# Optimization experiments

Measured on AMD Instinct MI355X. Metric: run time of the kernel, lower is better.

## Reference

```python
import jax, jax.numpy as jnp
import numpy as np

SAMPLING_RATIO = 1.0


def gcn_conv(x, src, dst, ew, W, b):
    """PyG GCNConv: h = D^-1/2 (A+I) D^-1/2 (xW) + b, edges weighted by ew.
    Masked edges (ew=0) contribute neither messages nor degree, exactly
    matching running the conv on the subset edge_index."""
    n = x.shape[0]
    h = x @ W                                              # [N, out]
    deg = jax.ops.segment_sum(ew, dst, num_segments=n) + 1.0  # +1 for self-loop
    dinv = jax.lax.rsqrt(deg)                              # deg >= 1, safe
    norm = dinv[src] * dinv[dst] * ew                      # [E]
    agg = jax.ops.segment_sum(h[src] * norm[:, None], dst, num_segments=n)
    return agg + h * (dinv * dinv)[:, None] + b            # self-loop term + bias


def setup_inputs() -> dict:
    key = jax.random.key(0)
    ks = jax.random.split(key, 8)
    N, E, F_IN, HID, OUT = 50000, 800000, 128, 128, 64
    x = jax.random.normal(ks[0], (N, F_IN), dtype=jnp.float32)
    edge_index = jax.random.randint(ks[1], (2, E), 0, N, dtype=jnp.int32)
    edge_rand = jax.random.uniform(ks[2], (E,), dtype=jnp.float32)
    s0 = 1.0 / np.sqrt(F_IN)
    s1 = 1.0 / np.sqrt(HID)
    w0 = jax.random.normal(ks[3], (F_IN, HID), dtype=jnp.float32) * s0
    b0 = jnp.zeros((HID,), dtype=jnp.float32)
    w1 = jax.random.normal(ks[4], (HID, HID), dtype=jnp.float32) * s1
    b1 = jnp.zeros((HID,), dtype=jnp.float32)
    w2 = jax.random.normal(ks[5], (HID, OUT), dtype=jnp.float32) * s1
    b2 = jnp.zeros((OUT,), dtype=jnp.float32)
    return {"x": x, "edge_index": edge_index, "edge_rand": edge_rand,
            "w0": w0, "b0": b0, "w1": w1, "b1": b1, "w2": w2, "b2": b2}


def reference(x, edge_index, edge_rand, w0, b0, w1, b1, w2, b2):
    src, dst = edge_index[0], edge_index[1]
    ones = jnp.ones(src.shape, dtype=x.dtype)
    # first pass over full graph -> tmp_z
    z = jax.nn.relu(gcn_conv(x, src, dst, ones, w0, b0))
    z = jax.nn.relu(gcn_conv(z, src, dst, ones, w1, b1))
    tmp_z = gcn_conv(z, src, dst, ones, w2, b2)
    # edge sampling: gather-dot-sigmoid-threshold (detached mask)
    edge_logit = jnp.sum(tmp_z[src] * tmp_z[dst], axis=-1)
    edge_weight = jax.nn.sigmoid(edge_logit)
    mask = jax.lax.stop_gradient(
        (edge_weight > SAMPLING_RATIO * edge_rand).astype(x.dtype))
    # second pass: sampled edges for hidden layers, full edges for last layer
    h = jax.nn.relu(gcn_conv(x, src, dst, mask, w0, b0))
    h = jax.nn.relu(gcn_conv(h, src, dst, mask, w1, b1))
    out = gcn_conv(h, src, dst, ones, w2, b2)
    return out
```

## Files before the change

kernel.cpp:

```cpp
#include <hip/hip_runtime.h>


typedef __attribute__((ext_vector_type(8))) short bf16x8;
typedef __attribute__((ext_vector_type(4))) float f32x4;

__device__ inline unsigned bfpair(float lo, float hi) {
    unsigned a = __float_as_uint(lo), b = __float_as_uint(hi);
    a = (a + 0x7FFFu + ((a >> 16) & 1u)) >> 16;
    b = (b + 0x7FFFu + ((b >> 16) & 1u)) & 0xFFFF0000u;
    return a | b;
}
__device__ inline unsigned short bf1(float v) {
    unsigned u = __float_as_uint(v);
    return (unsigned short)((u + 0x7FFFu + ((u >> 16) & 1u)) >> 16);
}
__device__ inline void unpack2(unsigned u, float& f0, float& f1) {
    f0 = __uint_as_float(u << 16);
    f1 = __uint_as_float(u & 0xFFFF0000u);
}

__global__ void k_scan1(const int* __restrict__ in, int* __restrict__ out,
                        int* __restrict__ bsums, int N) {
    __shared__ int tmp[256];
    int i = blockIdx.x * 256 + threadIdx.x;
    int v = (i < N) ? in[i] : 0;
    tmp[threadIdx.x] = v;
    __syncthreads();
    for (int off = 1; off < 256; off <<= 1) {
        int t = (threadIdx.x >= off) ? tmp[threadIdx.x - off] : 0;
        __syncthreads();
        tmp[threadIdx.x] += t;
        __syncthreads();
    }
    if (i < N) out[i] = tmp[threadIdx.x] - v;
    if (threadIdx.x == 255) bsums[blockIdx.x] = tmp[255];
}

__global__ void k_scan2(int* __restrict__ bsums, int nb) {
    __shared__ int tmp[256];
    int v = (threadIdx.x < nb) ? bsums[threadIdx.x] : 0;
    tmp[threadIdx.x] = v;
    __syncthreads();
    for (int off = 1; off < 256; off <<= 1) {
        int t = (threadIdx.x >= off) ? tmp[threadIdx.x - off] : 0;
        __syncthreads();
        tmp[threadIdx.x] += t;
        __syncthreads();
    }
    if (threadIdx.x < nb) bsums[threadIdx.x] = tmp[threadIdx.x] - v;
}

__global__ void k_scan3(int* __restrict__ out, const int* __restrict__ bsums, int N, int E) {
    int i = blockIdx.x * 256 + threadIdx.x;
    if (i < N) out[i] += bsums[blockIdx.x];
    if (i == 0) out[N] = E;
}

__global__ __launch_bounds__(256) void k_bcount(const int* __restrict__ dst,
                                                int* __restrict__ cnt, int E, int chunk) {
    __shared__ int h[1024];
    for (int i = threadIdx.x; i < 1024; i += 256) h[i] = 0;
    __syncthreads();
    int beg = blockIdx.x * chunk, end = min(E, beg + chunk);
    for (int e = beg + threadIdx.x; e < end; e += 256)
        atomicAdd(&h[dst[e] >> 6], 1);
    __syncthreads();
    for (int b = threadIdx.x; b < 1024; b += 256)
        cnt[b * 64 + blockIdx.x] = h[b];
}

__global__ __launch_bounds__(256) void k_bscatter(const int* __restrict__ src,
                                                  const int* __restrict__ dst,
                                                  const float* __restrict__ er,
                                                  const int* __restrict__ sbase,
                                                  int2* __restrict__ stg, int E, int chunk) {
    __shared__ int cur[1024];
    for (int i = threadIdx.x; i < 1024; i += 256) cur[i] = 0;
    __syncthreads();
    int beg = blockIdx.x * chunk, end = min(E, beg + chunk);
    for (int e = beg + threadIdx.x; e < end; e += 256) {
        int d = dst[e];
        int b = d >> 6;
        int loc = atomicAdd(&cur[b], 1);
        int pos = sbase[b * 64 + blockIdx.x] + loc;
        stg[pos] = make_int2(src[e] | ((d & 63) << 16), (int)__float_as_uint(er[e]));
    }
}

__global__ __launch_bounds__(256) void k_bindeg(const int2* __restrict__ stg,
                                                const int* __restrict__ sbase,
                                                int* __restrict__ indeg,
                                                float* __restrict__ dinvF, int N) {
    __shared__ int cnt[64];
    if (threadIdx.x < 64) cnt[threadIdx.x] = 0;
    __syncthreads();
    int b = blockIdx.x;
    int beg = sbase[b * 64], end = sbase[(b + 1) * 64];
    for (int i = beg + threadIdx.x; i < end; i += 256)
        atomicAdd(&cnt[(stg[i].x >> 16) & 63], 1);
    __syncthreads();
    if (threadIdx.x < 64) {
        int node = b * 64 + threadIdx.x;
        if (node < N) {
            int c = cnt[threadIdx.x];
            indeg[node] = c;
            dinvF[node] = 1.0f / sqrtf((float)c + 1.0f);
        }
    }
}

__global__ __launch_bounds__(256) void k_bfill(const int2* __restrict__ stg,
                                               const int* __restrict__ sbase,
                                               const int* __restrict__ csr_off,
                                               int2* __restrict__ csr_se, int N) {
    __shared__ int cur[64];
    int b = blockIdx.x;
    if (threadIdx.x < 64) {
        int node = b * 64 + threadIdx.x;
        cur[threadIdx.x] = (node < N) ? csr_off[node] : 0;
    }
    __syncthreads();
    int beg = sbase[b * 64], end = sbase[(b + 1) * 64];
    for (int i = beg + threadIdx.x; i < end; i += 256) {
        int2 se = stg[i];
        int j = (se.x >> 16) & 63;
        int pos = atomicAdd(&cur[j], 1);
        csr_se[pos] = make_int2(se.x & 0xFFFF, se.y);
    }
}

__global__ __launch_bounds__(128) void k_surv(const float* __restrict__ tz,
                                              const int* __restrict__ csr_off,
                                              const int2* __restrict__ csr_se,
                                              float* __restrict__ survive,
                                              float* __restrict__ dinvM, int N) {
    const int v = blockIdx.x;
    const int l = threadIdx.x & 15;
    const int s = threadIdx.x >> 4;
    const int e0 = csr_off[v];
    const int e1 = csr_off[v + 1];
    const float4 tv = *(const float4*)&tz[(size_t)v * 64 + l * 4];
    int cnt = 0;
    for (int i = e0 + s; i < e1; i += 8) {
        int2 se = csr_se[i];
        const float4 a = *(const float4*)&tz[(size_t)se.x * 64 + l * 4];
        float p = a.x * tv.x + a.y * tv.y + a.z * tv.z + a.w * tv.w;
        p += __shfl_xor(p, 1, 16);
        p += __shfl_xor(p, 2, 16);
        p += __shfl_xor(p, 4, 16);
        p += __shfl_xor(p, 8, 16);
        float sg = 1.0f / (1.0f + expf(-p));
        float m = (sg > __uint_as_float((unsigned)se.y)) ? 1.0f : 0.0f;
        if (l == 0) {
            survive[i] = m;
            cnt += (m != 0.0f) ? 1 : 0;
        }
    }
    __shared__ int sc[8];
    if (l == 0) sc[s] = cnt;
    __syncthreads();
    if (threadIdx.x == 0) {
        int t = 0;
#pragma unroll
        for (int k = 0; k < 8; k++) t += sc[k];
        dinvM[v] = 1.0f / sqrtf((float)t + 1.0f);
    }
}

__device__ inline void packw3_one(const float* __restrict__ W, unsigned short* __restrict__ Wp,
                                  int OUTC, int idx) {
    int l = idx & 63;
    int tk = idx >> 6;
    int kb = tk & 3;
    int ct = tk >> 2;
    size_t PL = (size_t)(OUTC / 16) * 4 * 64 * 8;
    unsigned short v0[8], v1[8], v2[8];
#pragma unroll
    for (int i = 0; i < 8; i++) {
        float wv = W[(kb * 32 + ((l >> 4) * 8) + i) * OUTC + ct * 16 + (l & 15)];
        unsigned short h0 = bf1(wv);
        float f0 = __uint_as_float((unsigned)h0 << 16);
        float r1 = wv - f0;
        unsigned short h1 = bf1(r1);
        float f1 = __uint_as_float((unsigned)h1 << 16);
        unsigned short h2 = bf1(r1 - f1);
        v0[i] = h0; v1[i] = h1; v2[i] = h2;
    }
    auto st = [](unsigned short* dst, unsigned short* v) {
        uint4 u;
        u.x = v[0] | ((unsigned)v[1] << 16);
        u.y = v[2] | ((unsigned)v[3] << 16);
        u.z = v[4] | ((unsigned)v[5] << 16);
        u.w = v[6] | ((unsigned)v[7] << 16);
        *(uint4*)dst = u;
    };
    st(&Wp[(size_t)idx * 8], v0);
    st(&Wp[PL + (size_t)idx * 8], v1);
    st(&Wp[2 * PL + (size_t)idx * 8], v2);
}

__global__ void k_packw3_all(const float* __restrict__ w0, const float* __restrict__ w1,
                             const float* __restrict__ w2,
                             unsigned short* __restrict__ w0p, unsigned short* __restrict__ w1p,
                             unsigned short* __restrict__ w2p) {
    int b = blockIdx.x;
    if (b < 8) packw3_one(w0, w0p, 128, b * 256 + threadIdx.x);
    else if (b < 16) packw3_one(w1, w1p, 128, (b - 8) * 256 + threadIdx.x);
    else packw3_one(w2, w2p, 64, (b - 16) * 256 + threadIdx.x);
}

template <int OUTC, bool WB16>
__global__ __launch_bounds__(256) void k_gemm_split(const float* __restrict__ A,
                                                    const unsigned short* __restrict__ Wp,
                                                    float* __restrict__ Cout,
                                                    unsigned short* __restrict__ Cb, int N) {
    constexpr int CT = OUTC / 16;
    constexpr int PL = CT * 4 * 64 * 8;
    constexpr int LDW = OUTC + 4;
    __shared__ float eps[64 * LDW];
    const int w = threadIdx.x >> 6;
    const int l = threadIdx.x & 63;
    int row = blockIdx.x * 64 + w * 16 + (l & 15);
    int rowc = (row < N) ? row : (N - 1);

    bf16x8 a0[4], a1[4], a2[4];
#pragma unroll
    for (int kb = 0; kb < 4; kb++) {
        const float* pa = &A[(size_t)rowc * 128 + kb * 32 + ((l >> 4) * 8)];
        float4 x0 = *(const float4*)pa;
        float4 x1 = *(const float4*)(pa + 4);
        float xa[8] = {x0.x, x0.y, x0.z, x0.w, x1.x, x1.y, x1.z, x1.w};
#pragma unroll
        for (int i = 0; i < 8; i++) {
            unsigned short h0 = bf1(xa[i]);
            float f0 = __uint_as_float((unsigned)h0 << 16);
            float r1 = xa[i] - f0;
            unsigned short h1 = bf1(r1);
            float f1 = __uint_as_float((unsigned)h1 << 16);
            unsigned short h2 = bf1(r1 - f1);
            a0[kb][i] = (short)h0;
            a1[kb][i] = (short)h1;
            a2[kb][i] = (short)h2;
        }
    }
#pragma unroll
    for (int ct = 0; ct < CT; ct++) {
        f32x4 accA = {0.f, 0.f, 0.f, 0.f};
        f32x4 accB = {0.f, 0.f, 0.f, 0.f};
#pragma unroll
        for (int kb = 0; kb < 4; kb++) {
            const size_t bo = ((size_t)(ct * 4 + kb) * 64 + l) * 8;
            bf16x8 b0 = *(const bf16x8*)&Wp[bo];
            bf16x8 b1 = *(const bf16x8*)&Wp[PL + bo];
            bf16x8 b2 = *(const bf16x8*)&Wp[2 * PL + bo];
            accA = __builtin_amdgcn_mfma_f32_16x16x32_bf16(a0[kb], b0, accA, 0, 0, 0);
            accB = __builtin_amdgcn_mfma_f32_16x16x32_bf16(a0[kb], b1, accB, 0, 0, 0);
            accA = __builtin_amdgcn_mfma_f32_16x16x32_bf16(a1[kb], b0, accA, 0, 0, 0);
            accB = __builtin_amdgcn_mfma_f32_16x16x32_bf16(a1[kb], b1, accB, 0, 0, 0);
            accA = __builtin_amdgcn_mfma_f32_16x16x32_bf16(a2[kb], b0, accA, 0, 0, 0);
            accB = __builtin_amdgcn_mfma_f32_16x16x32_bf16(a0[kb], b2, accB, 0, 0, 0);
        }
#pragma unroll
        for (int r = 0; r < 4; r++) {
            int rr = w * 16 + (l >> 4) * 4 + r;
            eps[rr * LDW + ct * 16 + (l & 15)] = accA[r] + accB[r];
        }
    }
    __syncthreads();
    constexpr int NF4 = 64 * OUTC / 4;
    for (int idx = threadIdx.x; idx < NF4; idx += 256) {
        int rl = idx / (OUTC / 4);
        int cg = idx % (OUTC / 4);
        int grow = blockIdx.x * 64 + rl;
        if (grow < N) {
            const float* sp = &eps[rl * LDW + cg * 4];
            float4 vv = make_float4(sp[0], sp[1], sp[2], sp[3]);
            *(float4*)&Cout[(size_t)grow * OUTC + cg * 4] = vv;
            if (WB16)
                *(uint2*)&Cb[(size_t)grow * OUTC + cg * 4] =
                    make_uint2(bfpair(vv.x, vv.y), bfpair(vv.z, vv.w));
        }
    }
}

template <int OUTC>
__global__ __launch_bounds__(256) void k_gemm_mfma(const unsigned short* __restrict__ A,
                                                   const unsigned short* __restrict__ Wpk,
                                                   unsigned short* __restrict__ C, int N) {
    constexpr int CT = OUTC / 16;
    __shared__ unsigned short eps[64 * OUTC];
    const int w = threadIdx.x >> 6;
    const int l = threadIdx.x & 63;
    const int rowl = (w * 16) + (l & 15);
    int row = blockIdx.x * 64 + rowl;
    int rowc = (row < N) ? row : (N - 1);

    bf16x8 a[4];
#pragma unroll
    for (int kb = 0; kb < 4; kb++)
        a[kb] = *(const bf16x8*)&A[(size_t)rowc * 128 + kb * 32 + ((l >> 4) * 8)];

#pragma unroll
    for (int ct = 0; ct < CT; ct++) {
        f32x4 acc = {0.f, 0.f, 0.f, 0.f};
#pragma unroll
        for (int kb = 0; kb < 4; kb++) {
            bf16x8 b = *(const bf16x8*)&Wpk[((size_t)(ct * 4 + kb) * 64 + l) * 8];
            acc = __builtin_amdgcn_mfma_f32_16x16x32_bf16(a[kb], b, acc, 0, 0, 0);
        }
#pragma unroll
        for (int r = 0; r < 4; r++) {
            int rr = w * 16 + (l >> 4) * 4 + r;
            eps[rr * OUTC + ct * 16 + (l & 15)] = bf1(acc[r]);
        }
    }
    __syncthreads();
    constexpr int NU4 = 64 * OUTC / 8;
    for (int idx = threadIdx.x; idx < NU4; idx += 256) {
        int rl = idx / (OUTC / 8);
        int cg = idx % (OUTC / 8);
        int grow = blockIdx.x * 64 + rl;
        if (grow < N)
            *(uint4*)&C[(size_t)grow * OUTC + cg * 8] = *(const uint4*)&eps[rl * OUTC + cg * 8];
    }
}

template <bool RELU>
__global__ __launch_bounds__(256) void k_agg128(const float* __restrict__ h,
                                                const int* __restrict__ csr_off,
                                                const int2* __restrict__ csr_se,
                                                const float* __restrict__ dinv,
                                                const float* __restrict__ bias,
                                                float* __restrict__ out, int N) {
    const int v = blockIdx.x * 4 + (threadIdx.x >> 6);
    if (v >= N) return;
    const int lane = threadIdx.x & 63;
    const int l = lane & 31;
    const int s = lane >> 5;
    const int e0 = csr_off[v];
    const int e1 = csr_off[v + 1];
    float4 acc = make_float4(0.f, 0.f, 0.f, 0.f);
    int i = e0 + s;
    for (; i + 2 < e1; i += 4) {
        int sa = csr_se[i].x;      float wa = dinv[sa];
        int sb = csr_se[i + 2].x;  float wb = dinv[sb];
        float4 a = *(const float4*)&h[(size_t)sa * 128 + l * 4];
        float4 b = *(const float4*)&h[(size_t)sb * 128 + l * 4];
        acc.x = fmaf(a.x, wa, acc.x); acc.y = fmaf(a.y, wa, acc.y);
        acc.z = fmaf(a.z, wa, acc.z); acc.w = fmaf(a.w, wa, acc.w);
        acc.x = fmaf(b.x, wb, acc.x); acc.y = fmaf(b.y, wb, acc.y);
        acc.z = fmaf(b.z, wb, acc.z); acc.w = fmaf(b.w, wb, acc.w);
    }
    if (i < e1) {
        int sa = csr_se[i].x;
        float wa = dinv[sa];
        float4 a = *(const float4*)&h[(size_t)sa * 128 + l * 4];
        acc.x = fmaf(a.x, wa, acc.x); acc.y = fmaf(a.y, wa, acc.y);
        acc.z = fmaf(a.z, wa, acc.z); acc.w = fmaf(a.w, wa, acc.w);
    }
    acc.x += __shfl_xor(acc.x, 32);
    acc.y += __shfl_xor(acc.y, 32);
    acc.z += __shfl_xor(acc.z, 32);
    acc.w += __shfl_xor(acc.w, 32);
    if (s == 0) {
        float dv = dinv[v];
        float4 hv = *(const float4*)&h[(size_t)v * 128 + l * 4];
        float4 bb = *(const float4*)&bias[l * 4];
        float4 o;
        o.x = dv * (acc.x + hv.x * dv) + bb.x;
        o.y = dv * (acc.y + hv.y * dv) + bb.y;
        o.z = dv * (acc.z + hv.z * dv) + bb.z;
        o.w = dv * (acc.w + hv.w * dv) + bb.w;
        if (RELU) {
            o.x = fmaxf(o.x, 0.f); o.y = fmaxf(o.y, 0.f);
            o.z = fmaxf(o.z, 0.f); o.w = fmaxf(o.w, 0.f);
        }
        *(float4*)&out[(size_t)v * 128 + l * 4] = o;
    }
}

__global__ __launch_bounds__(256) void k_agg64(const float* __restrict__ h,
                                               const int* __restrict__ csr_off,
                                               const int2* __restrict__ csr_se,
                                               const float* __restrict__ dinv,
                                               const float* __restrict__ bias,
                                               float* __restrict__ out, int N) {
    const int v = blockIdx.x * 4 + (threadIdx.x >> 6);
    if (v >= N) return;
    const int lane = threadIdx.x & 63;
    const int l = lane & 15;
    const int s = lane >> 4;
    const int e0 = csr_off[v];
    const int e1 = csr_off[v + 1];
    float4 acc = make_float4(0.f, 0.f, 0.f, 0.f);
    int i = e0 + s;
    for (; i + 4 < e1; i += 8) {
        int sa = csr_se[i].x;      float wa = dinv[sa];
        int sb = csr_se[i + 4].x;  float wb = dinv[sb];
        float4 a = *(const float4*)&h[(size_t)sa * 64 + l * 4];
        float4 b = *(const float4*)&h[(size_t)sb * 64 + l * 4];
        acc.x = fmaf(a.x, wa, acc.x); acc.y = fmaf(a.y, wa, acc.y);
        acc.z = fmaf(a.z, wa, acc.z); acc.w = fmaf(a.w, wa, acc.w);
        acc.x = fmaf(b.x, wb, acc.x); acc.y = fmaf(b.y, wb, acc.y);
        acc.z = fmaf(b.z, wb, acc.z); acc.w = fmaf(b.w, wb, acc.w);
    }
    if (i < e1) {
        int sa = csr_se[i].x;
        float wa = dinv[sa];
        float4 a = *(const float4*)&h[(size_t)sa * 64 + l * 4];
        acc.x = fmaf(a.x, wa, acc.x); acc.y = fmaf(a.y, wa, acc.y);
        acc.z = fmaf(a.z, wa, acc.z); acc.w = fmaf(a.w, wa, acc.w);
    }
    acc.x += __shfl_xor(acc.x, 32); acc.y += __shfl_xor(acc.y, 32);
    acc.z += __shfl_xor(acc.z, 32); acc.w += __shfl_xor(acc.w, 32);
    acc.x += __shfl_xor(acc.x, 16); acc.y += __shfl_xor(acc.y, 16);
    acc.z += __shfl_xor(acc.z, 16); acc.w += __shfl_xor(acc.w, 16);
    if (s == 0) {
        float dv = dinv[v];
        float4 hv = *(const float4*)&h[(size_t)v * 64 + l * 4];
        float4 bb = *(const float4*)&bias[l * 4];
        float4 o;
        o.x = dv * (acc.x + hv.x * dv) + bb.x;
        o.y = dv * (acc.y + hv.y * dv) + bb.y;
        o.z = dv * (acc.z + hv.z * dv) + bb.z;
        o.w = dv * (acc.w + hv.w * dv) + bb.w;
        *(float4*)&out[(size_t)v * 64 + l * 4] = o;
    }
}

template <bool RELU>
__global__ __launch_bounds__(256) void k_agg128b(const unsigned short* __restrict__ h,
                                                 const int* __restrict__ csr_off,
                                                 const int2* __restrict__ csr_se,
                                                 const float* __restrict__ survive,
                                                 const float* __restrict__ dinv,
                                                 const float* __restrict__ bias,
                                                 unsigned short* __restrict__ out, int N) {
    const int v = blockIdx.x * 4 + (threadIdx.x >> 6);
    if (v >= N) return;
    const int lane = threadIdx.x & 63;
    const int l = lane & 15;
    const int s = lane >> 4;
    const int e0 = csr_off[v];
    const int e1 = csr_off[v + 1];
    float acc[8];
#pragma unroll
    for (int j = 0; j < 8; j++) acc[j] = 0.f;
    int i = e0 + s;
    for (; i + 4 < e1; i += 8) {
        int sa = csr_se[i].x;
        int sb = csr_se[i + 4].x;
        float wa = dinv[sa] * survive[i];
        float wb = dinv[sb] * survive[i + 4];
        uint4 ua = *(const uint4*)&h[(size_t)sa * 128 + l * 8];
        uint4 ub = *(const uint4*)&h[(size_t)sb * 128 + l * 8];
        float f0, f1;
        unpack2(ua.x, f0, f1); acc[0] = fmaf(f0, wa, acc[0]); acc[1] = fmaf(f1, wa, acc[1]);
        unpack2(ua.y, f0, f1); acc[2] = fmaf(f0, wa, acc[2]); acc[3] = fmaf(f1, wa, acc[3]);
        unpack2(ua.z, f0, f1); acc[4] = fmaf(f0, wa, acc[4]); acc[5] = fmaf(f1, wa, acc[5]);
        unpack2(ua.w, f0, f1); acc[6] = fmaf(f0, wa, acc[6]); acc[7] = fmaf(f1, wa, acc[7]);
        unpack2(ub.x, f0, f1); acc[0] = fmaf(f0, wb, acc[0]); acc[1] = fmaf(f1, wb, acc[1]);
        unpack2(ub.y, f0, f1); acc[2] = fmaf(f0, wb, acc[2]); acc[3] = fmaf(f1, wb, acc[3]);
        unpack2(ub.z, f0, f1); acc[4] = fmaf(f0, wb, acc[4]); acc[5] = fmaf(f1, wb, acc[5]);
        unpack2(ub.w, f0, f1); acc[6] = fmaf(f0, wb, acc[6]); acc[7] = fmaf(f1, wb, acc[7]);
    }
    if (i < e1) {
        int sa = csr_se[i].x;
        float wa = dinv[sa] * survive[i];
        uint4 ua = *(const uint4*)&h[(size_t)sa * 128 + l * 8];
        float f0, f1;
        unpack2(ua.x, f0, f1); acc[0] = fmaf(f0, wa, acc[0]); acc[1] = fmaf(f1, wa, acc[1]);
        unpack2(ua.y, f0, f1); acc[2] = fmaf(f0, wa, acc[2]); acc[3] = fmaf(f1, wa, acc[3]);
        unpack2(ua.z, f0, f1); acc[4] = fmaf(f0, wa, acc[4]); acc[5] = fmaf(f1, wa, acc[5]);
        unpack2(ua.w, f0, f1); acc[6] = fmaf(f0, wa, acc[6]); acc[7] = fmaf(f1, wa, acc[7]);
    }
#pragma unroll
    for (int j = 0; j < 8; j++) acc[j] += __shfl_xor(acc[j], 32);
#pragma unroll
    for (int j = 0; j < 8; j++) acc[j] += __shfl_xor(acc[j], 16);
    if (s == 0) {
        float dv = dinv[v];
        uint4 uh = *(const uint4*)&h[(size_t)v * 128 + l * 8];
        float hv[8];
        unpack2(uh.x, hv[0], hv[1]); unpack2(uh.y, hv[2], hv[3]);
        unpack2(uh.z, hv[4], hv[5]); unpack2(uh.w, hv[6], hv[7]);
        unsigned u[4];
#pragma unroll
        for (int j2 = 0; j2 < 4; j2++) {
            float o0 = dv * (acc[2 * j2 + 0] + hv[2 * j2 + 0] * dv) + bias[l * 8 + 2 * j2 + 0];
            float o1 = dv * (acc[2 * j2 + 1] + hv[2 * j2 + 1] * dv) + bias[l * 8 + 2 * j2 + 1];
            if (RELU) { o0 = fmaxf(o0, 0.f); o1 = fmaxf(o1, 0.f); }
            u[j2] = bfpair(o0, o1);
        }
        *(uint4*)&out[(size_t)v * 128 + l * 8] = make_uint4(u[0], u[1], u[2], u[3]);
    }
}

__global__ __launch_bounds__(256) void k_agg64b(const unsigned short* __restrict__ h,
                                                const int* __restrict__ csr_off,
                                                const int2* __restrict__ csr_se,
                                                const float* __restrict__ dinv,
                                                const float* __restrict__ bias,
                                                float* __restrict__ out, int N) {
    const int v = blockIdx.x * 4 + (threadIdx.x >> 6);
    if (v >= N) return;
    const int lane = threadIdx.x & 63;
    const int l = lane & 7;
    const int s = lane >> 3;
    const int e0 = csr_off[v];
    const int e1 = csr_off[v + 1];
    float acc[8];
#pragma unroll
    for (int j = 0; j < 8; j++) acc[j] = 0.f;
    for (int i = e0 + s; i < e1; i += 8) {
        int sa = csr_se[i].x;
        float wa = dinv[sa];
        uint4 ua = *(const uint4*)&h[(size_t)sa * 64 + l * 8];
        float f0, f1;
        unpack2(ua.x, f0, f1); acc[0] = fmaf(f0, wa, acc[0]); acc[1] = fmaf(f1, wa, acc[1]);
        unpack2(ua.y, f0, f1); acc[2] = fmaf(f0, wa, acc[2]); acc[3] = fmaf(f1, wa, acc[3]);
        unpack2(ua.z, f0, f1); acc[4] = fmaf(f0, wa, acc[4]); acc[5] = fmaf(f1, wa, acc[5]);
        unpack2(ua.w, f0, f1); acc[6] = fmaf(f0, wa, acc[6]); acc[7] = fmaf(f1, wa, acc[7]);
    }
#pragma unroll
    for (int j = 0; j < 8; j++) acc[j] += __shfl_xor(acc[j], 32);
#pragma unroll
    for (int j = 0; j < 8; j++) acc[j] += __shfl_xor(acc[j], 16);
#pragma unroll
    for (int j = 0; j < 8; j++) acc[j] += __shfl_xor(acc[j], 8);
    if (s == 0) {
        float dv = dinv[v];
        uint4 uh = *(const uint4*)&h[(size_t)v * 64 + l * 8];
        float hv[8];
        unpack2(uh.x, hv[0], hv[1]); unpack2(uh.y, hv[2], hv[3]);
        unpack2(uh.z, hv[4], hv[5]); unpack2(uh.w, hv[6], hv[7]);
        float o[8];
#pragma unroll
        for (int j = 0; j < 8; j++) o[j] = dv * (acc[j] + hv[j] * dv) + bias[l * 8 + j];
        *(float4*)&out[(size_t)v * 64 + l * 8 + 0] = make_float4(o[0], o[1], o[2], o[3]);
        *(float4*)&out[(size_t)v * 64 + l * 8 + 4] = make_float4(o[4], o[5], o[6], o[7]);
    }
}

extern "C" void kernel_launch(void* const* d_in, const int* in_sizes, int n_in,
                              void* d_out, int out_size, void* d_ws, size_t ws_size,
                              hipStream_t stream) {
    const float* x  = (const float*)d_in[0];
    const int*   ei = (const int*)d_in[1];
    const float* er = (const float*)d_in[2];
    const float* w0 = (const float*)d_in[3];
    const float* b0 = (const float*)d_in[4];
    const float* w1 = (const float*)d_in[5];
    const float* b1 = (const float*)d_in[6];
    const float* w2 = (const float*)d_in[7];
    const float* b2 = (const float*)d_in[8];
    const int N = in_sizes[0] / 128;
    const int E = in_sizes[2];
    const int* src  = ei;
    const int* dstv = ei + E;
    float* out = (float*)d_out;

    char* p = (char*)d_ws;
    auto alloc = [&](size_t bytes) {
        char* r = p;
        p += (bytes + 255) & ~(size_t)255;
        return r;
    };
    int* indeg     = (int*)alloc((size_t)N * 4);
    int* csr_off   = (int*)alloc((size_t)(N + 1) * 4);
    int* bsums     = (int*)alloc(1024);
    int* bcnt      = (int*)alloc((size_t)65536 * 4);
    int* sbase     = (int*)alloc((size_t)65537 * 4);
    int2* csr_se   = (int2*)alloc((size_t)E * 8);
    int2* stg      = (int2*)alloc((size_t)E * 8);
    float* dinvF   = (float*)alloc((size_t)N * 4);
    float* dinvM   = (float*)alloc((size_t)N * 4);
    float* hx      = (float*)alloc((size_t)N * 128 * 4);
    unsigned short* hxb = (unsigned short*)alloc((size_t)N * 128 * 2);
    float* wk1     = (float*)alloc((size_t)N * 128 * 4);
    float* wk2     = (float*)alloc((size_t)N * 128 * 4);
    float* tz      = (float*)alloc((size_t)N * 64 * 4);
    unsigned short* w0p3 = (unsigned short*)alloc((size_t)3 * 128 * 128 * 2);
    unsigned short* w1p3 = (unsigned short*)alloc((size_t)3 * 128 * 128 * 2);
    unsigned short* w2p3 = (unsigned short*)alloc((size_t)3 * 128 * 64 * 2);
    unsigned short* wk1b = (unsigned short*)wk1;
    unsigned short* wk2b = (unsigned short*)wk2;
    float* survive = (float*)stg;

    const int nb = (N + 255) / 256;
    const int chunk = (E + 63) / 64;

    k_packw3_all<<<20, 256, 0, stream>>>(w0, w1, w2, w0p3, w1p3, w2p3);

    k_bcount<<<64, 256, 0, stream>>>(dstv, bcnt, E, chunk);
    k_scan1<<<256, 256, 0, stream>>>(bcnt, sbase, bsums, 65536);
    k_scan2<<<1, 256, 0, stream>>>(bsums, 256);
    k_scan3<<<256, 256, 0, stream>>>(sbase, bsums, 65536, E);
    k_bscatter<<<64, 256, 0, stream>>>(src, dstv, er, sbase, stg, E, chunk);
    k_bindeg<<<1024, 256, 0, stream>>>(stg, sbase, indeg, dinvF, N);
    k_scan1<<<nb, 256, 0, stream>>>(indeg, csr_off, bsums, N);
    k_scan2<<<1, 256, 0, stream>>>(bsums, nb);
    k_scan3<<<nb, 256, 0, stream>>>(csr_off, bsums, N, E);
    k_bfill<<<1024, 256, 0, stream>>>(stg, sbase, csr_off, csr_se, N);

    const int gbm = (N + 63) / 64;
    const int ga = (N + 3) / 4;

    k_gemm_split<128, true><<<gbm, 256, 0, stream>>>(x, w0p3, hx, hxb, N);

    k_agg128<true><<<ga, 256, 0, stream>>>(hx, csr_off, csr_se, dinvF, b0, wk1, N);
    k_gemm_split<128, false><<<gbm, 256, 0, stream>>>(wk1, w1p3, wk2, nullptr, N);
    k_agg128<true><<<ga, 256, 0, stream>>>(wk2, csr_off, csr_se, dinvF, b1, wk1, N);
    k_gemm_split<64, false><<<gbm, 256, 0, stream>>>(wk1, w2p3, wk2, nullptr, N);
    k_agg64<<<ga, 256, 0, stream>>>(wk2, csr_off, csr_se, dinvF, b2, tz, N);

    k_surv<<<N, 128, 0, stream>>>(tz, csr_off, csr_se, survive, dinvM, N);

    k_agg128b<true><<<ga, 256, 0, stream>>>(hxb, csr_off, csr_se, survive, dinvM, b0, wk1b, N);
    k_gemm_mfma<128><<<gbm, 256, 0, stream>>>(wk1b, w1p3, wk2b, N);
    k_agg128b<true><<<ga, 256, 0, stream>>>(wk2b, csr_off, csr_se, survive, dinvM, b1, wk1b, N);
    k_gemm_mfma<64><<<gbm, 256, 0, stream>>>(wk1b, w2p3, wk2b, N);
    k_agg64b<<<ga, 256, 0, stream>>>(wk2b, csr_off, csr_se, dinvF, b2, out, N);
}
```

Measured before the change: 462.5 us.

## Store node features in 16-column slices to improve gather cache locality

Changes intermediate feature matrices to a sliced layout where each group of 16 columns is stored contiguously for all nodes. Aggregation kernels are replaced by generic sliced kernels that launch one block per (node group, slice), gathering only a 64-byte (or 32-byte bf16) piece per neighbor. This shrinks the working set each slice touches so neighbor gathers hit L2/MALL more often. In exchange it multiplies grid size and repeats CSR/dinv reads per slice, and uses many more smaller random loads.

```diff
diff --git a/kernel.cpp b/kernel.cpp
--- a/kernel.cpp
+++ b/kernel.cpp
@@ -209,7 +209,7 @@
     else packw3_one(w2, w2p, 64, (b - 16) * 256 + threadIdx.x);
 }
 
-template <int OUTC, bool WB16>
+template <int OUTC, bool WB16, bool ASL>
 __global__ __launch_bounds__(256) void k_gemm_split(const float* __restrict__ A,
                                                     const unsigned short* __restrict__ Wp,
                                                     float* __restrict__ Cout,
@@ -226,7 +226,9 @@
     bf16x8 a0[4], a1[4], a2[4];
 #pragma unroll
     for (int kb = 0; kb < 4; kb++) {
-        const float* pa = &A[(size_t)rowc * 128 + kb * 32 + ((l >> 4) * 8)];
+        int col0 = kb * 32 + ((l >> 4) * 8);
+        const float* pa = ASL ? &A[((size_t)(col0 >> 4) * N + rowc) * 16 + (col0 & 15)]
+                              : &A[(size_t)rowc * 128 + col0];
         float4 x0 = *(const float4*)pa;
         float4 x1 = *(const float4*)(pa + 4);
         float xa[8] = {x0.x, x0.y, x0.z, x0.w, x1.x, x1.y, x1.z, x1.w};
@@ -275,10 +277,11 @@
         if (grow < N) {
             const float* sp = &eps[rl * LDW + cg * 4];
             float4 vv = make_float4(sp[0], sp[1], sp[2], sp[3]);
-            *(float4*)&Cout[(size_t)grow * OUTC + cg * 4] = vv;
+            int col0 = cg * 4;
+            size_t ad = ((size_t)(col0 >> 4) * N + grow) * 16 + (col0 & 15);
+            *(float4*)&Cout[ad] = vv;
             if (WB16)
-                *(uint2*)&Cb[(size_t)grow * OUTC + cg * 4] =
-                    make_uint2(bfpair(vv.x, vv.y), bfpair(vv.z, vv.w));
+                *(uint2*)&Cb[ad] = make_uint2(bfpair(vv.x, vv.y), bfpair(vv.z, vv.w));
         }
     }
 }
@@ -291,15 +294,15 @@
     __shared__ unsigned short eps[64 * OUTC];
     const int w = threadIdx.x >> 6;
     const int l = threadIdx.x & 63;
-    const int rowl = (w * 16) + (l & 15);
-    int row = blockIdx.x * 64 + rowl;
+    int row = blockIdx.x * 64 + (w * 16) + (l & 15);
     int rowc = (row < N) ? row : (N - 1);
 
     bf16x8 a[4];
 #pragma unroll
-    for (int kb = 0; kb < 4; kb++)
-        a[kb] = *(const bf16x8*)&A[(size_t)rowc * 128 + kb * 32 + ((l >> 4) * 8)];
-
+    for (int kb = 0; kb < 4; kb++) {
+        int col0 = kb * 32 + ((l >> 4) * 8);
+        a[kb] = *(const bf16x8*)&A[((size_t)(col0 >> 4) * N + rowc) * 16 + (col0 & 15)];
+    }
 #pragma unroll
     for (int ct = 0; ct < CT; ct++) {
         f32x4 acc = {0.f, 0.f, 0.f, 0.f};
@@ -320,52 +323,49 @@
         int rl = idx / (OUTC / 8);
         int cg = idx % (OUTC / 8);
         int grow = blockIdx.x * 64 + rl;
-        if (grow < N)
-            *(uint4*)&C[(size_t)grow * OUTC + cg * 8] = *(const uint4*)&eps[rl * OUTC + cg * 8];
-    }
-}
-
-template <bool RELU>
-__global__ __launch_bounds__(256) void k_agg128(const float* __restrict__ h,
-                                                const int* __restrict__ csr_off,
-                                                const int2* __restrict__ csr_se,
-                                                const float* __restrict__ dinv,
-                                                const float* __restrict__ bias,
-                                                float* __restrict__ out, int N) {
-    const int v = blockIdx.x * 4 + (threadIdx.x >> 6);
+        if (grow < N) {
+            size_t ad = ((size_t)(cg >> 1) * N + grow) * 16 + (cg & 1) * 8;
+            *(uint4*)&C[ad] = *(const uint4*)&eps[rl * OUTC + cg * 8];
+        }
+    }
+}
+
+template <int NSL, bool RELU, bool TZOUT>
+__global__ __launch_bounds__(256) void k_aggs(const float* __restrict__ hs,
+                                              const int* __restrict__ csr_off,
+                                              const int2* __restrict__ csr_se,
+                                              const float* __restrict__ dinv,
+                                              const float* __restrict__ bias,
+                                              float* __restrict__ outp, int N) {
+    const int s = blockIdx.x & (NSL - 1);
+    const int v = (blockIdx.x / NSL) * 4 + (threadIdx.x >> 6);
     if (v >= N) return;
     const int lane = threadIdx.x & 63;
-    const int l = lane & 31;
-    const int s = lane >> 5;
+    const int fl = lane & 3;
+    const int slot = lane >> 2;
     const int e0 = csr_off[v];
     const int e1 = csr_off[v + 1];
+    const size_t sb = (size_t)s * N;
     float4 acc = make_float4(0.f, 0.f, 0.f, 0.f);
-    int i = e0 + s;
-    for (; i + 2 < e1; i += 4) {
-        int sa = csr_se[i].x;      float wa = dinv[sa];
-        int sb = csr_se[i + 2].x;  float wb = dinv[sb];
-        float4 a = *(const float4*)&h[(size_t)sa * 128 + l * 4];
-        float4 b = *(const float4*)&h[(size_t)sb * 128 + l * 4];
+    for (int i = e0 + slot; i < e1; i += 16) {
+        int sa = csr_se[i].x;
+        float wa = dinv[sa];
+        float4 a = *(const float4*)&hs[(sb + sa) * 16 + fl * 4];
         acc.x = fmaf(a.x, wa, acc.x); acc.y = fmaf(a.y, wa, acc.y);
         acc.z = fmaf(a.z, wa, acc.z); acc.w = fmaf(a.w, wa, acc.w);
-        acc.x = fmaf(b.x, wb, acc.x); acc.y = fmaf(b.y, wb, acc.y);
-        acc.z = fmaf(b.z, wb, acc.z); acc.w = fmaf(b.w, wb, acc.w);
-    }
-    if (i < e1) {
-        int sa = csr_se[i].x;
-        float wa = dinv[sa];
-        float4 a = *(const float4*)&h[(size_t)sa * 128 + l * 4];
-        acc.x = fmaf(a.x, wa, acc.x); acc.y = fmaf(a.y, wa, acc.y);
-        acc.z = fmaf(a.z, wa, acc.z); acc.w = fmaf(a.w, wa, acc.w);
-    }
-    acc.x += __shfl_xor(acc.x, 32);
-    acc.y += __shfl_xor(acc.y, 32);
-    acc.z += __shfl_xor(acc.z, 32);
-    acc.w += __shfl_xor(acc.w, 32);
-    if (s == 0) {
+    }
+    acc.x += __shfl_xor(acc.x, 4);  acc.y += __shfl_xor(acc.y, 4);
+    acc.z += __shfl_xor(acc.z, 4);  acc.w += __shfl_xor(acc.w, 4);
+    acc.x += __shfl_xor(acc.x, 8);  acc.y += __shfl_xor(acc.y, 8);
+    acc.z += __shfl_xor(acc.z, 8);  acc.w += __shfl_xor(acc.w, 8);
+    acc.x += __shfl_xor(acc.x, 16); acc.y += __shfl_xor(acc.y, 16);
+    acc.z += __shfl_xor(acc.z, 16); acc.w += __shfl_xor(acc.w, 16);
+    acc.x += __shfl_xor(acc.x, 32); acc.y += __shfl_xor(acc.y, 32);
+    acc.z += __shfl_xor(acc.z, 32); acc.w += __shfl_xor(acc.w, 32);
+    if (slot == 0) {
         float dv = dinv[v];
-        float4 hv = *(const float4*)&h[(size_t)v * 128 + l * 4];
-        float4 bb = *(const float4*)&bias[l * 4];
+        float4 hv = *(const float4*)&hs[(sb + v) * 16 + fl * 4];
+        float4 bb = *(const float4*)&bias[s * 16 + fl * 4];
         float4 o;
         o.x = dv * (acc.x + hv.x * dv) + bb.x;
         o.y = dv * (acc.y + hv.y * dv) + bb.y;
@@ -375,170 +375,66 @@
             o.x = fmaxf(o.x, 0.f); o.y = fmaxf(o.y, 0.f);
             o.z = fmaxf(o.z, 0.f); o.w = fmaxf(o.w, 0.f);
         }
-        *(float4*)&out[(size_t)v * 128 + l * 4] = o;
-    }
-}
-
-__global__ __launch_bounds__(256) void k_agg64(const float* __restrict__ h,
+        if (TZOUT)
+            *(float4*)&outp[(size_t)v * (NSL * 16) + s * 16 + fl * 4] = o;
+        else
+            *(float4*)&outp[(sb + v) * 16 + fl * 4] = o;
+    }
+}
+
+template <int NSL, bool RELU, bool MASKED, bool F32OUT>
+__global__ __launch_bounds__(256) void k_aggsb(const unsigned short* __restrict__ hs,
                                                const int* __restrict__ csr_off,
                                                const int2* __restrict__ csr_se,
+                                               const float* __restrict__ survive,
                                                const float* __restrict__ dinv,
                                                const float* __restrict__ bias,
-                                               float* __restrict__ out, int N) {
-    const int v = blockIdx.x * 4 + (threadIdx.x >> 6);
+                                               void* __restrict__ outp, int N) {
+    const int s = blockIdx.x & (NSL - 1);
+    const int v = (blockIdx.x / NSL) * 4 + (threadIdx.x >> 6);
     if (v >= N) return;
     const int lane = threadIdx.x & 63;
-    const int l = lane & 15;
-    const int s = lane >> 4;
+    const int fl = lane & 3;
+    const int slot = lane >> 2;
     const int e0 = csr_off[v];
     const int e1 = csr_off[v + 1];
-    float4 acc = make_float4(0.f, 0.f, 0.f, 0.f);
-    int i = e0 + s;
-    for (; i + 4 < e1; i += 8) {
-        int sa = csr_se[i].x;      float wa = dinv[sa];
-        int sb = csr_se[i + 4].x;  float wb = dinv[sb];
-        float4 a = *(const float4*)&h[(size_t)sa * 64 + l * 4];
-        float4 b = *(const float4*)&h[(size_t)sb * 64 + l * 4];
-        acc.x = fmaf(a.x, wa, acc.x); acc.y = fmaf(a.y, wa, acc.y);
-        acc.z = fmaf(a.z, wa, acc.z); acc.w = fmaf(a.w, wa, acc.w);
-        acc.x = fmaf(b.x, wb, acc.x); acc.y = fmaf(b.y, wb, acc.y);
-        acc.z = fmaf(b.z, wb, acc.z); acc.w = fmaf(b.w, wb, acc.w);
-    }
-    if (i < e1) {
+    const size_t sb = (size_t)s * N;
+    float acc[4] = {0.f, 0.f, 0.f, 0.f};
+    for (int i = e0 + slot; i < e1; i += 16) {
         int sa = csr_se[i].x;
-        float wa = dinv[sa];
-        float4 a = *(const float4*)&h[(size_t)sa * 64 + l * 4];
-        acc.x = fmaf(a.x, wa, acc.x); acc.y = fmaf(a.y, wa, acc.y);
-        acc.z = fmaf(a.z, wa, acc.z); acc.w = fmaf(a.w, wa, acc.w);
-    }
-    acc.x += __shfl_xor(acc.x, 32); acc.y += __shfl_xor(acc.y, 32);
-    acc.z += __shfl_xor(acc.z, 32); acc.w += __shfl_xor(acc.w, 32);
-    acc.x += __shfl_xor(acc.x, 16); acc.y += __shfl_xor(acc.y, 16);
-    acc.z += __shfl_xor(acc.z, 16); acc.w += __shfl_xor(acc.w, 16);
-    if (s == 0) {
-        float dv = dinv[v];
-        float4 hv = *(const float4*)&h[(size_t)v * 64 + l * 4];
-        float4 bb = *(const float4*)&bias[l * 4];
-        float4 o;
-        o.x = dv * (acc.x + hv.x * dv) + bb.x;
-        o.y = dv * (acc.y + hv.y * dv) + bb.y;
-        o.z = dv * (acc.z + hv.z * dv) + bb.z;
-        o.w = dv * (acc.w + hv.w * dv) + bb.w;
-        *(float4*)&out[(size_t)v * 64 + l * 4] = o;
-    }
-}
-
-template <bool RELU>
-__global__ __launch_bounds__(256) void k_agg128b(const unsigned short* __restrict__ h,
-                                                 const int* __restrict__ csr_off,
-                                                 const int2* __restrict__ csr_se,
-                                                 const float* __restrict__ survive,
-                                                 const float* __restrict__ dinv,
-                                                 const float* __restrict__ bias,
-                                                 unsigned short* __restrict__ out, int N) {
-    const int v = blockIdx.x * 4 + (threadIdx.x >> 6);
-    if (v >= N) return;
-    const int lane = threadIdx.x & 63;
-    const int l = lane & 15;
-    const int s = lane >> 4;
-    const int e0 = csr_off[v];
-    const int e1 = csr_off[v + 1];
-    float acc[8];
-#pragma unroll
-    for (int j = 0; j < 8; j++) acc[j] = 0.f;
-    int i = e0 + s;
-    for (; i + 4 < e1; i += 8) {
-        int sa = csr_se[i].x;
-        int sb = csr_se[i + 4].x;
-        float wa = dinv[sa] * survive[i];
-        float wb = dinv[sb] * survive[i + 4];
-        uint4 ua = *(const uint4*)&h[(size_t)sa * 128 + l * 8];
-        uint4 ub = *(const uint4*)&h[(size_t)sb * 128 + l * 8];
+        float wa = MASKED ? dinv[sa] * survive[i] : dinv[sa];
+        uint2 ua = *(const uint2*)&hs[(sb + sa) * 16 + fl * 4];
         float f0, f1;
         unpack2(ua.x, f0, f1); acc[0] = fmaf(f0, wa, acc[0]); acc[1] = fmaf(f1, wa, acc[1]);
         unpack2(ua.y, f0, f1); acc[2] = fmaf(f0, wa, acc[2]); acc[3] = fmaf(f1, wa, acc[3]);
-        unpack2(ua.z, f0, f1); acc[4] = fmaf(f0, wa, acc[4]); acc[5] = fmaf(f1, wa, acc[5]);
-        unpack2(ua.w, f0, f1); acc[6] = fmaf(f0, wa, acc[6]); acc[7] = fmaf(f1, wa, acc[7]);
-        unpack2(ub.x, f0, f1); acc[0] = fmaf(f0, wb, acc[0]); acc[1] = fmaf(f1, wb, acc[1]);
-        unpack2(ub.y, f0, f1); acc[2] = fmaf(f0, wb, acc[2]); acc[3] = fmaf(f1, wb, acc[3]);
-        unpack2(ub.z, f0, f1); acc[4] = fmaf(f0, wb, acc[4]); acc[5] = fmaf(f1, wb, acc[5]);
-        unpack2(ub.w, f0, f1); acc[6] = fmaf(f0, wb, acc[6]); acc[7] = fmaf(f1, wb, acc[7]);
-    }
-    if (i < e1) {
-        int sa = csr_se[i].x;
-        float wa = dinv[sa] * survive[i];
-        uint4 ua = *(const uint4*)&h[(size_t)sa * 128 + l * 8];
-        float f0, f1;
-        unpack2(ua.x, f0, f1); acc[0] = fmaf(f0, wa, acc[0]); acc[1] = fmaf(f1, wa, acc[1]);
-        unpack2(ua.y, f0, f1); acc[2] = fmaf(f0, wa, acc[2]); acc[3] = fmaf(f1, wa, acc[3]);
-        unpack2(ua.z, f0, f1); acc[4] = fmaf(f0, wa, acc[4]); acc[5] = fmaf(f1, wa, acc[5]);
-        unpack2(ua.w, f0, f1); acc[6] = fmaf(f0, wa, acc[6]); acc[7] = fmaf(f1, wa, acc[7]);
-    }
-#pragma unroll
-    for (int j = 0; j < 8; j++) acc[j] += __shfl_xor(acc[j], 32);
-#pragma unroll
-    for (int j = 0; j < 8; j++) acc[j] += __shfl_xor(acc[j], 16);
-    if (s == 0) {
+    }
+#pragma unroll
+    for (int j = 0; j < 4; j++) acc[j] += __shfl_xor(acc[j], 4);
+#pragma unroll
+    for (int j = 0; j < 4; j++) acc[j] += __shfl_xor(acc[j], 8);
+#pragma unroll
+    for (int j = 0; j < 4; j++) acc[j] += __shfl_xor(acc[j], 16);
+#pragma unroll
+    for (int j = 0; j < 4; j++) acc[j] += __shfl_xor(acc[j], 32);
+    if (slot == 0) {
         float dv = dinv[v];
-        uint4 uh = *(const uint4*)&h[(size_t)v * 128 + l * 8];
-        float hv[8];
-        unpack2(uh.x, hv[0], hv[1]); unpack2(uh.y, hv[2], hv[3]);
-        unpack2(uh.z, hv[4], hv[5]); unpack2(uh.w, hv[6], hv[7]);
-        unsigned u[4];
-#pragma unroll
-        for (int j2 = 0; j2 < 4; j2++) {
-            float o0 = dv * (acc[2 * j2 + 0] + hv[2 * j2 + 0] * dv) + bias[l * 8 + 2 * j2 + 0];
-            float o1 = dv * (acc[2 * j2 + 1] + hv[2 * j2 + 1] * dv) + bias[l * 8 + 2 * j2 + 1];
-            if (RELU) { o0 = fmaxf(o0, 0.f); o1 = fmaxf(o1, 0.f); }
-            u[j2] = bfpair(o0, o1);
-        }
-        *(uint4*)&out[(size_t)v * 128 + l * 8] = make_uint4(u[0], u[1], u[2], u[3]);
-    }
-}
-
-__global__ __launch_bounds__(256) void k_agg64b(const unsigned short* __restrict__ h,
-                                                const int* __restrict__ csr_off,
-                                                const int2* __restrict__ csr_se,
-                                                const float* __restrict__ dinv,
-                                                const float* __restrict__ bias,
-                                                float* __restrict__ out, int N) {
-    const int v = blockIdx.x * 4 + (threadIdx.x >> 6);
-    if (v >= N) return;
-    const int lane = threadIdx.x & 63;
-    const int l = lane & 7;
-    const int s = lane >> 3;
-    const int e0 = csr_off[v];
-    const int e1 = csr_off[v + 1];
-    float acc[8];
-#pragma unroll
-    for (int j = 0; j < 8; j++) acc[j] = 0.f;
-    for (int i = e0 + s; i < e1; i += 8) {
-        int sa = csr_se[i].x;
-        float wa = dinv[sa];
-        uint4 ua = *(const uint4*)&h[(size_t)sa * 64 + l * 8];
-        float f0, f1;
-        unpack2(ua.x, f0, f1); acc[0] = fmaf(f0, wa, acc[0]); acc[1] = fmaf(f1, wa, acc[1]);
-        unpack2(ua.y, f0, f1); acc[2] = fmaf(f0, wa, acc[2]); acc[3] = fmaf(f1, wa, acc[3]);
-        unpack2(ua.z, f0, f1); acc[4] = fmaf(f0, wa, acc[4]); acc[5] = fmaf(f1, wa, acc[5]);
-        unpack2(ua.w, f0, f1); acc[6] = fmaf(f0, wa, acc[6]); acc[7] = fmaf(f1, wa, acc[7]);
-    }
-#pragma unroll
-    for (int j = 0; j < 8; j++) acc[j] += __shfl_xor(acc[j], 32);
-#pragma unroll
-    for (int j = 0; j < 8; j++) acc[j] += __shfl_xor(acc[j], 16);
-#pragma unroll
-    for (int j = 0; j < 8; j++) acc[j] += __shfl_xor(acc[j], 8);
-    if (s == 0) {
-        float dv = dinv[v];
-        uint4 uh = *(const uint4*)&h[(size_t)v * 64 + l * 8];
-        float hv[8];
-        unpack2(uh.x, hv[0], hv[1]); unpack2(uh.y, hv[2], hv[3]);
-        unpack2(uh.z, hv[4], hv[5]); unpack2(uh.w, hv[6], hv[7]);
-        float o[8];
-#pragma unroll
-        for (int j = 0; j < 8; j++) o[j] = dv * (acc[j] + hv[j] * dv) + bias[l * 8 + j];
-        *(float4*)&out[(size_t)v * 64 + l * 8 + 0] = make_float4(o[0], o[1], o[2], o[3]);
-        *(float4*)&out[(size_t)v * 64 + l * 8 + 4] = make_float4(o[4], o[5], o[6], o[7]);
+        uint2 uh = *(const uint2*)&hs[(sb + v) * 16 + fl * 4];
+        float hv[4];
+        unpack2(uh.x, hv[0], hv[1]);
+        unpack2(uh.y, hv[2], hv[3]);
+        float o[4];
+#pragma unroll
+        for (int j = 0; j < 4; j++) {
+            o[j] = dv * (acc[j] + hv[j] * dv) + bias[s * 16 + fl * 4 + j];
+            if (RELU) o[j] = fmaxf(o[j], 0.f);
+        }
+        if (F32OUT) {
+            *(float4*)&((float*)outp)[(size_t)v * (NSL * 16) + s * 16 + fl * 4] =
+                make_float4(o[0], o[1], o[2], o[3]);
+        } else {
+            *(uint2*)&((unsigned short*)outp)[(sb + v) * 16 + fl * 4] =
+                make_uint2(bfpair(o[0], o[1]), bfpair(o[2], o[3]));
+        }
     }
 }
 
@@ -604,21 +500,23 @@
     k_bfill<<<1024, 256, 0, stream>>>(stg, sbase, csr_off, csr_se, N);
 
     const int gbm = (N + 63) / 64;
-    const int ga = (N + 3) / 4;
-
-    k_gemm_split<128, true><<<gbm, 256, 0, stream>>>(x, w0p3, hx, hxb, N);
-
-    k_agg128<true><<<ga, 256, 0, stream>>>(hx, csr_off, csr_se, dinvF, b0, wk1, N);
-    k_gemm_split<128, false><<<gbm, 256, 0, stream>>>(wk1, w1p3, wk2, nullptr, N);
-    k_agg128<true><<<ga, 256, 0, stream>>>(wk2, csr_off, csr_se, dinvF, b1, wk1, N);
-    k_gemm_split<64, false><<<gbm, 256, 0, stream>>>(wk1, w2p3, wk2, nullptr, N);
-    k_agg64<<<ga, 256, 0, stream>>>(wk2, csr_off, csr_se, dinvF, b2, tz, N);
+    const int gn4 = (N + 3) / 4;
+    const int ga8 = gn4 * 8;
+    const int ga4 = gn4 * 4;
+
+    k_gemm_split<128, true, false><<<gbm, 256, 0, stream>>>(x, w0p3, hx, hxb, N);
+
+    k_aggs<8, true, false><<<ga8, 256, 0, stream>>>(hx, csr_off, csr_se, dinvF, b0, wk1, N);
+    k_gemm_split<128, false, true><<<gbm, 256, 0, stream>>>(wk1, w1p3, wk2, nullptr, N);
+    k_aggs<8, true, false><<<ga8, 256, 0, stream>>>(wk2, csr_off, csr_se, dinvF, b1, wk1, N);
+    k_gemm_split<64, false, true><<<gbm, 256, 0, stream>>>(wk1, w2p3, wk2, nullptr, N);
+    k_aggs<4, false, true><<<ga4, 256, 0, stream>>>(wk2, csr_off, csr_se, dinvF, b2, tz, N);
 
     k_surv<<<N, 128, 0, stream>>>(tz, csr_off, csr_se, survive, dinvM, N);
 
-    k_agg128b<true><<<ga, 256, 0, stream>>>(hxb, csr_off, csr_se, survive, dinvM, b0, wk1b, N);
+    k_aggsb<8, true, true, false><<<ga8, 256, 0, stream>>>(hxb, csr_off, csr_se, survive, dinvM, b0, wk1b, N);
     k_gemm_mfma<128><<<gbm, 256, 0, stream>>>(wk1b, w1p3, wk2b, N);
-    k_agg128b<true><<<ga, 256, 0, stream>>>(wk2b, csr_off, csr_se, survive, dinvM, b1, wk1b, N);
+    k_aggsb<8, true, true, false><<<ga8, 256, 0, stream>>>(wk2b, csr_off, csr_se, survive, dinvM, b1, wk1b, N);
     k_gemm_mfma<64><<<gbm, 256, 0, stream>>>(wk1b, w2p3, wk2b, N);
-    k_agg64b<<<ga, 256, 0, stream>>>(wk2b, csr_off, csr_se, dinvF, b2, out, N);
-}
+    k_aggsb<4, false, false, true><<<ga4, 256, 0, stream>>>(wk2b, csr_off, csr_se, survive, dinvF, b2, out, N);
+}
```

New measurement: 822.1 us. 77.8% more time.
